# Kernel optimization log

Measured on AMD Instinct MI355X. Metric: run time of the kernel, lower is better.

The kernel has to match this reference:

```python
import jax, jax.numpy as jnp
import numpy as np

N = 50000
E = 800000
DIN = 128
DH = 128
DOUT = 10
G = 128  # number of graphs in the batch


def gcn_conv(x, W, b, src, dst, n):
    """PyG GCNConv: self-loops + symmetric normalization + scatter-add."""
    loops = jnp.arange(n, dtype=src.dtype)
    s = jnp.concatenate([src, loops])
    d = jnp.concatenate([dst, loops])
    deg = jax.ops.segment_sum(jnp.ones_like(d, dtype=x.dtype), d, num_segments=n)
    dinv = jax.lax.rsqrt(deg)  # deg >= 1 because of self-loops
    norm = dinv[s] * dinv[d]  # [E+N]
    h = x @ W  # [n, out]
    msg = h[s] * norm[:, None]  # gather + scale
    out = jax.ops.segment_sum(msg, d, num_segments=n)  # scatter-add
    return out + b


def setup_inputs() -> dict:
    key = jax.random.key(0)
    ks = jax.random.split(key, 12)
    x = jax.random.normal(ks[0], (N, DIN), dtype=jnp.float32)
    edge_index = jax.random.randint(ks[1], (2, E), 0, N, dtype=jnp.int64)
    batch = jnp.sort(jax.random.randint(ks[2], (N,), 0, G, dtype=jnp.int64))
    def glorot(k, fan_in, fan_out):
        lim = np.sqrt(6.0 / (fan_in + fan_out)).astype(np.float32)
        return jax.random.uniform(k, (fan_in, fan_out), jnp.float32, -lim, lim)
    W1 = glorot(ks[3], DIN, DH); b1 = jnp.zeros((DH,), jnp.float32)
    W2 = glorot(ks[4], DH, DH); b2 = jnp.zeros((DH,), jnp.float32)
    W3 = glorot(ks[5], DH, DH); b3 = jnp.zeros((DH,), jnp.float32)
    Wl = glorot(ks[6], DH, DOUT); bl = jnp.zeros((DOUT,), jnp.float32)
    return {"x": x, "edge_index": edge_index, "batch": batch,
            "W1": W1, "b1": b1, "W2": W2, "b2": b2, "W3": W3, "b3": b3,
            "Wl": Wl, "bl": bl}


def reference(x, edge_index, batch, W1, b1, W2, b2, W3, b3, Wl, bl):
    src, dst = edge_index[0], edge_index[1]
    h = gcn_conv(x, W1, b1, src, dst, N)
    h = jax.nn.relu(h)  # dropout is identity at inference
    h = gcn_conv(h, W2, b2, src, dst, N)
    h = jax.nn.relu(h)
    h = gcn_conv(h, W3, b3, src, dst, N)
    # global mean pool over graphs
    sums = jax.ops.segment_sum(h, batch, num_segments=G)  # [G, DH]
    cnts = jax.ops.segment_sum(jnp.ones((N,), h.dtype), batch, num_segments=G)
    pooled = sums / jnp.maximum(cnts, 1.0)[:, None]
    logits = pooled @ Wl + bl
    return jax.nn.log_softmax(logits, axis=-1)
```

## Files before the change

kernel.cpp:

```cpp
#include <hip/hip_runtime.h>

#define NN 50000
#define NE 800000
#define DHID 128
#define NGR 128
#define DOUT 10
#define CSR_LDS_CAP 128

__device__ __forceinline__ int padcap(int cnt) { return ((cnt + 3) >> 2) << 2; }

template <int SEL>
__device__ __forceinline__ float fp8_dec(int word) {
    return __builtin_amdgcn_cvt_f32_fp8(word, SEL);
}


__global__ void k_init(int* deg, int* cursor, float* gsum) {
    int i = blockIdx.x * blockDim.x + threadIdx.x;
    if (i < NN) { deg[i] = 1; cursor[i] = 0; }
    if (i < NGR * DHID) gsum[i] = 0.f;
}

__global__ void k_count(const int* __restrict__ dst, int* __restrict__ deg) {
    int e = blockIdx.x * blockDim.x + threadIdx.x;
    if (e < NE) atomicAdd(&deg[dst[e]], 1);
}

__global__ void k_scanA(const int* __restrict__ deg, float* __restrict__ dinv,
                        int* __restrict__ bsum) {
    __shared__ int sm[256];
    int t = threadIdx.x;
    int i = blockIdx.x * 256 + t;
    int d = (i < NN) ? deg[i] : 1;
    if (i < NN) dinv[i] = rsqrtf((float)d);
    sm[t] = padcap(d - 1);
    __syncthreads();
    for (int o = 128; o > 0; o >>= 1) {
        if (t < o) sm[t] += sm[t + o];
        __syncthreads();
    }
    if (t == 0) bsum[blockIdx.x] = sm[0];
}

__global__ void k_scanB(int* bsum, int nb) {
    __shared__ int sm[256];
    int t = threadIdx.x;
    int v = (t < nb) ? bsum[t] : 0;
    sm[t] = v;
    __syncthreads();
    for (int o = 1; o < 256; o <<= 1) {
        int x = (t >= o) ? sm[t - o] : 0;
        __syncthreads();
        sm[t] += x;
        __syncthreads();
    }
    if (t < nb) bsum[t] = sm[t] - v;
}

__global__ void k_scanC(const int* __restrict__ deg, const int* __restrict__ bsum,
                        int* __restrict__ offs) {
    __shared__ int sm[256];
    int t = threadIdx.x;
    int i = blockIdx.x * 256 + t;
    int c = (i < NN) ? padcap(deg[i] - 1) : 0;
    sm[t] = c;
    __syncthreads();
    for (int o = 1; o < 256; o <<= 1) {
        int x = (t >= o) ? sm[t - o] : 0;
        __syncthreads();
        sm[t] += x;
        __syncthreads();
    }
    if (i < NN) offs[i] = bsum[blockIdx.x] + sm[t] - c;
}

__global__ void k_fill(const int* __restrict__ src, const int* __restrict__ dst,
                       const int* __restrict__ offs, int* __restrict__ cursor,
                       const float* __restrict__ dinv,
                       int2* __restrict__ csr) {
    int e = blockIdx.x * blockDim.x + threadIdx.x;
    if (e >= NE) return;
    int s = src[e], d = dst[e];
    int p = offs[d] + atomicAdd(&cursor[d], 1);
    csr[p] = make_int2(s, __float_as_int(dinv[s] * dinv[d]));
}

__global__ void k_pad(const int* __restrict__ deg, const int* __restrict__ offs,
                      int2* __restrict__ csr) {
    int i = blockIdx.x * blockDim.x + threadIdx.x;
    if (i >= NN) return;
    int cnt = deg[i] - 1;
    int cap = padcap(cnt);
    int base = offs[i];
    for (int p = cnt; p < cap; p++) csr[base + p] = make_int2(0, 0);
}

__global__ __launch_bounds__(256) void k_gemm(const float* __restrict__ X,
                                              const float* __restrict__ W,
                                              unsigned int* __restrict__ C8) {
    __shared__ float Xs[16][68];
    __shared__ float Ws[16][128];
    int t = threadIdx.x;
    int tx = t & 15, ty = t >> 4;
    int rowBase = blockIdx.x * 64;

    float acc[4][8];
#pragma unroll
    for (int i = 0; i < 4; i++)
#pragma unroll
        for (int j = 0; j < 8; j++) acc[i][j] = 0.f;

    for (int kk = 0; kk < 128; kk += 16) {
        {
            int r = t >> 2, q = t & 3;
            int grow = rowBase + r;
            float4 v = make_float4(0.f, 0.f, 0.f, 0.f);
            if (grow < NN)
                v = *reinterpret_cast<const float4*>(&X[grow * 128 + kk + 4 * q]);
            Xs[4 * q + 0][r] = v.x;
            Xs[4 * q + 1][r] = v.y;
            Xs[4 * q + 2][r] = v.z;
            Xs[4 * q + 3][r] = v.w;
        }
#pragma unroll
        for (int rep = 0; rep < 2; rep++) {
            int idx = t + rep * 256;
            int k = idx >> 5, c4 = idx & 31;
            *reinterpret_cast<float4*>(&Ws[k][4 * c4]) =
                *reinterpret_cast<const float4*>(&W[(kk + k) * 128 + 4 * c4]);
        }
        __syncthreads();
#pragma unroll
        for (int k = 0; k < 16; k++) {
            float4 xv = *reinterpret_cast<const float4*>(&Xs[k][4 * ty]);
            float4 w0 = *reinterpret_cast<const float4*>(&Ws[k][8 * tx]);
            float4 w1 = *reinterpret_cast<const float4*>(&Ws[k][8 * tx + 4]);
            float xa[4] = {xv.x, xv.y, xv.z, xv.w};
            float wa[8] = {w0.x, w0.y, w0.z, w0.w, w1.x, w1.y, w1.z, w1.w};
#pragma unroll
            for (int i = 0; i < 4; i++)
#pragma unroll
                for (int j = 0; j < 8; j++) acc[i][j] += xa[i] * wa[j];
        }
        __syncthreads();
    }
#pragma unroll
    for (int i = 0; i < 4; i++) {
        int grow = rowBase + 4 * ty + i;
        if (grow < NN) {
            int lo = __builtin_amdgcn_cvt_pk_fp8_f32(acc[i][0], acc[i][1], 0, false);
            lo = __builtin_amdgcn_cvt_pk_fp8_f32(acc[i][2], acc[i][3], lo, true);
            int hi = __builtin_amdgcn_cvt_pk_fp8_f32(acc[i][4], acc[i][5], 0, false);
            hi = __builtin_amdgcn_cvt_pk_fp8_f32(acc[i][6], acc[i][7], hi, true);
            *reinterpret_cast<uint2*>(&C8[(size_t)grow * 32 + 2 * tx]) =
                make_uint2((unsigned)lo, (unsigned)hi);
        }
    }
}

__global__ __launch_bounds__(256) void k_agg(const unsigned short* __restrict__ feat,
                                             const int2* __restrict__ csr,
                                             const int* __restrict__ offs,
                                             const int* __restrict__ deg,
                                             const float* __restrict__ dinv,
                                             const float* __restrict__ bias,
                                             float* __restrict__ out, int relu,
                                             const int* __restrict__ batch,
                                             float* __restrict__ gsum, int do_pool) {
    __shared__ int2 smCsr[4][CSR_LDS_CAP];
    int wid = threadIdx.x >> 6;
    int lane = threadIdx.x & 63;
    int node = blockIdx.x * 4 + wid;
    if (node >= NN) return;
    float di = dinv[node];
    int v = feat[(size_t)node * 64 + lane];
    float w0 = di * di;
    float2 a0 = make_float2(w0 * fp8_dec<0>(v), w0 * fp8_dec<1>(v));
    float2 a1 = make_float2(0.f, 0.f);
    float2 a2 = make_float2(0.f, 0.f);
    float2 a3 = make_float2(0.f, 0.f);
    int start = offs[node];
    int cap = padcap(deg[node] - 1);
    int capL = min(cap, CSR_LDS_CAP);

    for (int i = lane; i < capL; i += 64) smCsr[wid][i] = csr[start + i];

    int e = 0;
    for (; e + 8 <= capL; e += 8) {
        int2 p[8];
#pragma unroll
        for (int j = 0; j < 8; j++) p[j] = smCsr[wid][e + j];
        int u[8];
#pragma unroll
        for (int j = 0; j < 8; j++) u[j] = feat[(size_t)p[j].x * 64 + lane];
#pragma unroll
        for (int j = 0; j < 8; j++) {
            float w = __int_as_float(p[j].y);
            float ux = fp8_dec<0>(u[j]), uy = fp8_dec<1>(u[j]);
            if ((j & 3) == 0) { a0.x += w * ux; a0.y += w * uy; }
            if ((j & 3) == 1) { a1.x += w * ux; a1.y += w * uy; }
            if ((j & 3) == 2) { a2.x += w * ux; a2.y += w * uy; }
            if ((j & 3) == 3) { a3.x += w * ux; a3.y += w * uy; }
        }
    }
    if (e < capL) {
        int2 p[4];
#pragma unroll
        for (int j = 0; j < 4; j++) p[j] = smCsr[wid][e + j];
        int u[4];
#pragma unroll
        for (int j = 0; j < 4; j++) u[j] = feat[(size_t)p[j].x * 64 + lane];
#pragma unroll
        for (int j = 0; j < 4; j++) {
            float w = __int_as_float(p[j].y);
            float ux = fp8_dec<0>(u[j]), uy = fp8_dec<1>(u[j]);
            if (j == 0) { a0.x += w * ux; a0.y += w * uy; }
            if (j == 1) { a1.x += w * ux; a1.y += w * uy; }
            if (j == 2) { a2.x += w * ux; a2.y += w * uy; }
            if (j == 3) { a3.x += w * ux; a3.y += w * uy; }
        }
    }
    for (int q = capL; q < cap; q += 4) {
        int2 p[4];
#pragma unroll
        for (int j = 0; j < 4; j++) p[j] = csr[start + q + j];
#pragma unroll
        for (int j = 0; j < 4; j++) {
            float w = __int_as_float(p[j].y);
            int u = feat[(size_t)p[j].x * 64 + lane];
            a0.x += w * fp8_dec<0>(u);
            a0.y += w * fp8_dec<1>(u);
        }
    }

    float2 acc = make_float2(a0.x + a1.x + a2.x + a3.x, a0.y + a1.y + a2.y + a3.y);
    float2 b = reinterpret_cast<const float2*>(bias)[lane];
    acc.x += b.x;
    acc.y += b.y;
    if (relu) {
        acc.x = fmaxf(acc.x, 0.f);
        acc.y = fmaxf(acc.y, 0.f);
    }
    if (do_pool) {
        int g = batch[node];
        atomicAdd(&gsum[g * DHID + 2 * lane + 0], acc.x);
        atomicAdd(&gsum[g * DHID + 2 * lane + 1], acc.y);
    } else {
        reinterpret_cast<float2*>(out)[(size_t)node * 64 + lane] = acc;
    }
}

__global__ __launch_bounds__(128) void k_head(const float* __restrict__ gsum,
                                              const int* __restrict__ batch,
                                              const float* __restrict__ Wl,
                                              const float* __restrict__ bl,
                                              float* __restrict__ out) {
    __shared__ float pooled[128];
    __shared__ float logits[DOUT];
    int g = blockIdx.x;
    int t = threadIdx.x;
    int lo = 0, hi = NN;
    while (lo < hi) {
        int m = (lo + hi) >> 1;
        if (batch[m] < g) lo = m + 1;
        else hi = m;
    }
    int a = lo, b = NN;
    while (a < b) {
        int m = (a + b) >> 1;
        if (batch[m] < g + 1) a = m + 1;
        else b = m;
    }
    int cnt = a - lo;
    pooled[t] = gsum[g * DHID + t] / (float)max(cnt, 1);
    __syncthreads();
    if (t < DOUT) {
        float acc = bl[t];
        for (int k = 0; k < 128; k++) acc += pooled[k] * Wl[k * DOUT + t];
        logits[t] = acc;
    }
    __syncthreads();
    if (t < DOUT) {
        float m = -1e30f;
        for (int j = 0; j < DOUT; j++) m = fmaxf(m, logits[j]);
        float se = 0.f;
        for (int j = 0; j < DOUT; j++) se += expf(logits[j] - m);
        out[g * DOUT + t] = logits[t] - m - logf(se);
    }
}

extern "C" void kernel_launch(void* const* d_in, const int* in_sizes, int n_in,
                              void* d_out, int out_size, void* d_ws, size_t ws_size,
                              hipStream_t stream) {
    const float* x  = (const float*)d_in[0];
    const int*   ei = (const int*)d_in[1];
    const int* batch = (const int*)d_in[2];
    const float* W1 = (const float*)d_in[3];
    const float* b1 = (const float*)d_in[4];
    const float* W2 = (const float*)d_in[5];
    const float* b2 = (const float*)d_in[6];
    const float* W3 = (const float*)d_in[7];
    const float* b3 = (const float*)d_in[8];
    const float* Wl = (const float*)d_in[9];
    const float* bl = (const float*)d_in[10];
    float* out = (float*)d_out;

    const int* src = ei;
    const int* dst = ei + NE;

    char* ws = (char*)d_ws;
    size_t off = 0;
    auto alloc = [&](size_t bytes) {
        void* p = ws + off;
        off += (bytes + 255) / 256 * 256;
        return p;
    };
    int*   deg     = (int*)alloc(NN * 4);
    int*   cursor  = (int*)alloc(NN * 4);
    float* dinv    = (float*)alloc(NN * 4);
    int*   offs    = (int*)alloc(NN * 4);
    int*   bsum    = (int*)alloc(1024);
    float* gsum    = (float*)alloc(NGR * DHID * 4);
    int2*  csr     = (int2*)alloc((size_t)(NE + 4 * NN) * 8);
    unsigned int* h8 = (unsigned int*)alloc((size_t)NN * 128);
    float* A       = (float*)alloc((size_t)NN * 128 * 4);

    int nb = (NN + 255) / 256;
    k_init<<<nb, 256, 0, stream>>>(deg, cursor, gsum);
    k_count<<<NE / 256, 256, 0, stream>>>(dst, deg);
    k_scanA<<<nb, 256, 0, stream>>>(deg, dinv, bsum);
    k_scanB<<<1, 256, 0, stream>>>(bsum, nb);
    k_scanC<<<nb, 256, 0, stream>>>(deg, bsum, offs);
    k_fill<<<NE / 256, 256, 0, stream>>>(src, dst, offs, cursor, dinv, csr);
    k_pad<<<nb, 256, 0, stream>>>(deg, offs, csr);

    int gB = (NN + 63) / 64;
    const unsigned short* h16 = (const unsigned short*)h8;
    k_gemm<<<gB, 256, 0, stream>>>(x, W1, h8);
    k_agg<<<NN / 4, 256, 0, stream>>>(h16, csr, offs, deg, dinv, b1, A, 1,
                                      batch, gsum, 0);
    k_gemm<<<gB, 256, 0, stream>>>(A, W2, h8);
    k_agg<<<NN / 4, 256, 0, stream>>>(h16, csr, offs, deg, dinv, b2, A, 1,
                                      batch, gsum, 0);
    k_gemm<<<gB, 256, 0, stream>>>(A, W3, h8);
    k_agg<<<NN / 4, 256, 0, stream>>>(h16, csr, offs, deg, dinv, b3, A, 0,
                                      batch, gsum, 1);
    k_head<<<NGR, 128, 0, stream>>>(gsum, batch, Wl, bl, out);
}
```

Baseline: 419.9 us.

## Split each wavefront into two half-waves gathering different neighbors with 4-byte loads

The aggregation kernel now has each 64-lane wavefront split into two 32-lane halves. Each half processes alternate neighbor edges, and each lane loads 4 fp8 features (32-bit) instead of 2 (16-bit). The two halves' partial sums are combined with a cross-half shuffle, and only the first half writes a float4 of output or does the pooling atomics. This halves the number of gather instructions per edge and doubles the edges in flight per iteration. In exchange it adds a shuffle reduction and leaves half the lanes idle in the epilogue.

```diff
diff --git a/kernel.cpp b/kernel.cpp
--- a/kernel.cpp
+++ b/kernel.cpp
@@ -158,7 +158,7 @@
     }
 }
 
-__global__ __launch_bounds__(256) void k_agg(const unsigned short* __restrict__ feat,
+__global__ __launch_bounds__(256) void k_agg(const unsigned int* __restrict__ feat,
                                              const int2* __restrict__ csr,
                                              const int* __restrict__ offs,
                                              const int* __restrict__ deg,
@@ -172,81 +172,89 @@
     int lane = threadIdx.x & 63;
     int node = blockIdx.x * 4 + wid;
     if (node >= NN) return;
-    float di = dinv[node];
-    int v = feat[(size_t)node * 64 + lane];
-    float w0 = di * di;
-    float2 a0 = make_float2(w0 * fp8_dec<0>(v), w0 * fp8_dec<1>(v));
-    float2 a1 = make_float2(0.f, 0.f);
-    float2 a2 = make_float2(0.f, 0.f);
-    float2 a3 = make_float2(0.f, 0.f);
+    int half = lane >> 5;
+    int hl = lane & 31;
+
     int start = offs[node];
     int cap = padcap(deg[node] - 1);
     int capL = min(cap, CSR_LDS_CAP);
-
     for (int i = lane; i < capL; i += 64) smCsr[wid][i] = csr[start + i];
 
+    float di = dinv[node];
+    float wself = (half == 0) ? di * di : 0.f;
+    unsigned int sv = feat[(size_t)node * 32 + hl];
+    float p0[4] = {wself * fp8_dec<0>(sv), wself * fp8_dec<1>(sv),
+                   wself * fp8_dec<2>(sv), wself * fp8_dec<3>(sv)};
+    float p1[4] = {0.f, 0.f, 0.f, 0.f};
+
+#define ACC4(A, W, U)                                                     \
+    do {                                                                  \
+        (A)[0] += (W) * fp8_dec<0>(U);                                    \
+        (A)[1] += (W) * fp8_dec<1>(U);                                    \
+        (A)[2] += (W) * fp8_dec<2>(U);                                    \
+        (A)[3] += (W) * fp8_dec<3>(U);                                    \
+    } while (0)
+
     int e = 0;
-    for (; e + 8 <= capL; e += 8) {
-        int2 p[8];
-#pragma unroll
-        for (int j = 0; j < 8; j++) p[j] = smCsr[wid][e + j];
-        int u[8];
-#pragma unroll
-        for (int j = 0; j < 8; j++) u[j] = feat[(size_t)p[j].x * 64 + lane];
+    for (; e + 16 <= capL; e += 16) {
+        int2 r[8];
+#pragma unroll
+        for (int j = 0; j < 8; j++) r[j] = smCsr[wid][e + 2 * j + half];
+        unsigned int u[8];
+#pragma unroll
+        for (int j = 0; j < 8; j++) u[j] = feat[(size_t)r[j].x * 32 + hl];
 #pragma unroll
         for (int j = 0; j < 8; j++) {
-            float w = __int_as_float(p[j].y);
-            float ux = fp8_dec<0>(u[j]), uy = fp8_dec<1>(u[j]);
-            if ((j & 3) == 0) { a0.x += w * ux; a0.y += w * uy; }
-            if ((j & 3) == 1) { a1.x += w * ux; a1.y += w * uy; }
-            if ((j & 3) == 2) { a2.x += w * ux; a2.y += w * uy; }
-            if ((j & 3) == 3) { a3.x += w * ux; a3.y += w * uy; }
-        }
-    }
-    if (e < capL) {
-        int2 p[4];
-#pragma unroll
-        for (int j = 0; j < 4; j++) p[j] = smCsr[wid][e + j];
-        int u[4];
-#pragma unroll
-        for (int j = 0; j < 4; j++) u[j] = feat[(size_t)p[j].x * 64 + lane];
-#pragma unroll
-        for (int j = 0; j < 4; j++) {
-            float w = __int_as_float(p[j].y);
-            float ux = fp8_dec<0>(u[j]), uy = fp8_dec<1>(u[j]);
-            if (j == 0) { a0.x += w * ux; a0.y += w * uy; }
-            if (j == 1) { a1.x += w * ux; a1.y += w * uy; }
-            if (j == 2) { a2.x += w * ux; a2.y += w * uy; }
-            if (j == 3) { a3.x += w * ux; a3.y += w * uy; }
-        }
+            float w = __int_as_float(r[j].y);
+            if (j & 1) ACC4(p1, w, u[j]);
+            else       ACC4(p0, w, u[j]);
+        }
+    }
+    for (; e < capL; e += 4) {
+        int2 r0 = smCsr[wid][e + half];
+        int2 r1 = smCsr[wid][e + 2 + half];
+        unsigned int u0 = feat[(size_t)r0.x * 32 + hl];
+        unsigned int u1 = feat[(size_t)r1.x * 32 + hl];
+        float wA = __int_as_float(r0.y);
+        float wB = __int_as_float(r1.y);
+        ACC4(p0, wA, u0);
+        ACC4(p1, wB, u1);
     }
     for (int q = capL; q < cap; q += 4) {
-        int2 p[4];
-#pragma unroll
-        for (int j = 0; j < 4; j++) p[j] = csr[start + q + j];
-#pragma unroll
-        for (int j = 0; j < 4; j++) {
-            float w = __int_as_float(p[j].y);
-            int u = feat[(size_t)p[j].x * 64 + lane];
-            a0.x += w * fp8_dec<0>(u);
-            a0.y += w * fp8_dec<1>(u);
-        }
-    }
-
-    float2 acc = make_float2(a0.x + a1.x + a2.x + a3.x, a0.y + a1.y + a2.y + a3.y);
-    float2 b = reinterpret_cast<const float2*>(bias)[lane];
-    acc.x += b.x;
-    acc.y += b.y;
-    if (relu) {
-        acc.x = fmaxf(acc.x, 0.f);
-        acc.y = fmaxf(acc.y, 0.f);
-    }
-    if (do_pool) {
-        int g = batch[node];
-        atomicAdd(&gsum[g * DHID + 2 * lane + 0], acc.x);
-        atomicAdd(&gsum[g * DHID + 2 * lane + 1], acc.y);
-    } else {
-        reinterpret_cast<float2*>(out)[(size_t)node * 64 + lane] = acc;
+        int2 r0 = csr[start + q + half];
+        int2 r1 = csr[start + q + 2 + half];
+        unsigned int u0 = feat[(size_t)r0.x * 32 + hl];
+        unsigned int u1 = feat[(size_t)r1.x * 32 + hl];
+        float wA = __int_as_float(r0.y);
+        float wB = __int_as_float(r1.y);
+        ACC4(p0, wA, u0);
+        ACC4(p1, wB, u1);
+    }
+#undef ACC4
+
+    float a[4];
+#pragma unroll
+    for (int k = 0; k < 4; k++) {
+        a[k] = p0[k] + p1[k];
+        a[k] += __shfl_xor(a[k], 32, 64);
+    }
+
+    if (half == 0) {
+        float4 b = reinterpret_cast<const float4*>(bias)[hl];
+        a[0] += b.x; a[1] += b.y; a[2] += b.z; a[3] += b.w;
+        if (relu) {
+#pragma unroll
+            for (int k = 0; k < 4; k++) a[k] = fmaxf(a[k], 0.f);
+        }
+        if (do_pool) {
+            int g = batch[node];
+#pragma unroll
+            for (int k = 0; k < 4; k++)
+                atomicAdd(&gsum[g * DHID + 4 * hl + k], a[k]);
+        } else {
+            reinterpret_cast<float4*>(out + (size_t)node * 128)[hl] =
+                make_float4(a[0], a[1], a[2], a[3]);
+        }
     }
 }
 
@@ -335,15 +343,14 @@
     k_pad<<<nb, 256, 0, stream>>>(deg, offs, csr);
 
     int gB = (NN + 63) / 64;
-    const unsigned short* h16 = (const unsigned short*)h8;
     k_gemm<<<gB, 256, 0, stream>>>(x, W1, h8);
-    k_agg<<<NN / 4, 256, 0, stream>>>(h16, csr, offs, deg, dinv, b1, A, 1,
+    k_agg<<<NN / 4, 256, 0, stream>>>(h8, csr, offs, deg, dinv, b1, A, 1,
                                       batch, gsum, 0);
     k_gemm<<<gB, 256, 0, stream>>>(A, W2, h8);
-    k_agg<<<NN / 4, 256, 0, stream>>>(h16, csr, offs, deg, dinv, b2, A, 1,
+    k_agg<<<NN / 4, 256, 0, stream>>>(h8, csr, offs, deg, dinv, b2, A, 1,
                                       batch, gsum, 0);
     k_gemm<<<gB, 256, 0, stream>>>(A, W3, h8);
-    k_agg<<<NN / 4, 256, 0, stream>>>(h16, csr, offs, deg, dinv, b3, A, 0,
+    k_agg<<<NN / 4, 256, 0, stream>>>(h8, csr, offs, deg, dinv, b3, A, 0,
                                       batch, gsum, 1);
     k_head<<<NGR, 128, 0, stream>>>(gsum, batch, Wl, bl, out);
 }
```

Result: slower. 492.7 us (+17.3%).
